# Kernel tuning notes

Measured on AMD Instinct MI355X. Metric: run time of the kernel, lower is better.

The kernel has to match this reference:

```python
import jax, jax.numpy as jnp
import numpy as np

B, N, D, H = 1, 4096, 768, 12
HD = D // H
SCALE = HD ** -0.5

def setup_inputs() -> dict:
    key = jax.random.key(0)
    k1, k2, k3 = jax.random.split(key, 3)
    x = jax.random.normal(k1, (B, N, D), dtype=jnp.float32)
    W_qkv = jax.random.normal(k2, (D, 3 * D), dtype=jnp.float32) * (D ** -0.5)
    W_out = jax.random.normal(k3, (D, D), dtype=jnp.float32) * (D ** -0.5)
    b_out = jnp.zeros((D,), dtype=jnp.float32)
    return {"x": x, "W_qkv": W_qkv, "W_out": W_out, "b_out": b_out}

def reference(x, W_qkv, W_out, b_out):
    # qkv projection: (B,N,3D)
    qkv = x @ W_qkv
    q, k, v = jnp.split(qkv, 3, axis=-1)
    # (B,N,D) -> (B,H,N,hd)
    def heads(t):
        return t.reshape(B, N, H, HD).transpose(0, 2, 1, 3)
    q, k, v = heads(q), heads(k), heads(v)
    scores = jnp.einsum('bhnd,bhmd->bhnm', q, k) * SCALE  # (B,H,N,N)
    attn = jax.nn.softmax(scores, axis=-1)
    out = jnp.einsum('bhnm,bhmd->bhnd', attn, v)
    out = out.transpose(0, 2, 1, 3).reshape(B, N, D)
    return out @ W_out + b_out
```

## Files before the change

kernel.cpp:

```cpp
#include <hip/hip_runtime.h>
#include <hip/hip_bf16.h>
#include <math.h>

typedef __attribute__((ext_vector_type(8))) short bf16x8;
typedef __attribute__((ext_vector_type(4))) short bf16x4;
typedef __attribute__((ext_vector_type(4))) float floatx4;

constexpr int kN  = 4096;
constexpr int kD  = 768;
constexpr int kH  = 12;
constexpr int kHD = 64;
constexpr int k3D = 2304;
constexpr float kQScale = 0.18033688011112042f;

static __device__ __forceinline__ short f2b(float f) {
    __hip_bfloat16 h = __float2bfloat16(f);
    return *reinterpret_cast<short*>(&h);
}

static __device__ __forceinline__ float fast_exp2(float x) {
#if __has_builtin(__builtin_amdgcn_exp2f)
    return __builtin_amdgcn_exp2f(x);
#else
    return exp2f(x);
#endif
}

static __device__ __forceinline__ void async_copy16(const void* g, void* l) {
    __builtin_amdgcn_global_load_lds(
        (const __attribute__((address_space(1))) void*)g,
        (__attribute__((address_space(3))) void*)l, 16, 0, 0);
}

constexpr int kBlkX  = 1536;
constexpr int kBlkWq = 72 * 24;
constexpr int kBlkWo = 24 * 24;

__global__ __launch_bounds__(256)
void prep(const float* __restrict__ x, const float* __restrict__ Wq,
          const float* __restrict__ Wo, short* __restrict__ Xb,
          short* __restrict__ WqT, short* __restrict__ WoT)
{
    const int bid = blockIdx.x;
    const int tid = threadIdx.x;
    if (bid < kBlkX) {
        const int i = bid * 256 + tid;
        const float4* s = reinterpret_cast<const float4*>(x + (size_t)i * 8);
        float4 a = s[0], b = s[1];
        bf16x8 v;
        v[0] = f2b(a.x); v[1] = f2b(a.y); v[2] = f2b(a.z); v[3] = f2b(a.w);
        v[4] = f2b(b.x); v[5] = f2b(b.y); v[6] = f2b(b.z); v[7] = f2b(b.w);
        *reinterpret_cast<bf16x8*>(Xb + (size_t)i * 8) = v;
        return;
    }
    const float* src; short* dst; int R, C, bx, by;
    if (bid < kBlkX + kBlkWq) {
        const int local = bid - kBlkX;
        src = Wq; dst = WqT; R = kD; C = k3D; bx = local % 72; by = local / 72;
    } else {
        const int local = bid - kBlkX - kBlkWq;
        src = Wo; dst = WoT; R = kD; C = kD; bx = local % 24; by = local / 24;
    }
    __shared__ float t[32][33];
    const int c0 = bx * 32, r0 = by * 32;
    const int tx = tid & 31, ty = tid >> 5;
    #pragma unroll
    for (int i = ty; i < 32; i += 8)
        t[i][tx] = src[(size_t)(r0 + i) * C + c0 + tx];
    __syncthreads();
    #pragma unroll
    for (int i = ty; i < 32; i += 8)
        dst[(size_t)(c0 + i) * R + r0 + tx] = f2b(t[tx][i]);
}

template<int MODE>
__device__ __forceinline__
void gemm_core(const short* __restrict__ A, const short* __restrict__ BT,
               const float* __restrict__ bias, float* __restrict__ Cout,
               short* __restrict__ Qh, short* __restrict__ Kh, short* __restrict__ Vt,
               int N, int K)
{
    const int bm   = blockIdx.x * 128;
    const int bn   = blockIdx.y * 128;
    const int tid  = threadIdx.x;
    const int wave = tid >> 6;
    const int lane = tid & 63;
    const int l15  = lane & 15;
    const int quad = lane >> 4;
    const int l3   = l15 & 3;

    __shared__ alignas(16) short As[128 * 32];
    __shared__ alignas(16) short Bs[128 * 32];

    floatx4 acc[4][4] = {};
    const int wm = (wave >> 1) * 64;
    const int wn = (wave & 1) * 64;

    const int srl = lane >> 2;
    const int scc = (lane & 3) ^ (srl & 3);

    for (int k0 = 0; k0 < K; k0 += 32) {
        __syncthreads();
        #pragma unroll
        for (int j = 0; j < 2; ++j) {
            const int rs = 32 * wave + 16 * j;
            async_copy16(&A [(size_t)(bm + rs + srl) * K + k0 + 8 * scc], &As[rs * 32]);
            async_copy16(&BT[(size_t)(bn + rs + srl) * K + k0 + 8 * scc], &Bs[rs * 32]);
        }
        __syncthreads();

        bf16x8 af[4], bfr[4];
        #pragma unroll
        for (int mt = 0; mt < 4; ++mt)
            af[mt] = *reinterpret_cast<const bf16x8*>(&As[(wm + 16 * mt + l15) * 32 + 8 * (quad ^ l3)]);
        #pragma unroll
        for (int nt = 0; nt < 4; ++nt)
            bfr[nt] = *reinterpret_cast<const bf16x8*>(&Bs[(wn + 16 * nt + l15) * 32 + 8 * (quad ^ l3)]);
        #pragma unroll
        for (int mt = 0; mt < 4; ++mt)
            #pragma unroll
            for (int nt = 0; nt < 4; ++nt)
                acc[mt][nt] = __builtin_amdgcn_mfma_f32_16x16x32_bf16(af[mt], bfr[nt], acc[mt][nt], 0, 0, 0);
    }

    #pragma unroll
    for (int mt = 0; mt < 4; ++mt) {
        #pragma unroll
        for (int nt = 0; nt < 4; ++nt) {
            #pragma unroll
            for (int r = 0; r < 4; ++r) {
                const int row = bm + wm + mt * 16 + 4 * quad + r;
                const int col = bn + wn + nt * 16 + l15;
                float v = acc[mt][nt][r];
                if (MODE == 0) {
                    Cout[(size_t)row * N + col] = v + bias[col];
                } else {
                    const int proj   = col / kD;
                    const int within = col - proj * kD;
                    const int h = within >> 6;
                    const int d = within & 63;
                    if (proj == 0)      Qh[((size_t)h * kN + row) * kHD + d] = f2b(v * kQScale);
                    else if (proj == 1) Kh[((size_t)h * kN + row) * kHD + d] = f2b(v);
                    else                Vt[((size_t)h * kHD + d) * kN + row] = f2b(v);
                }
            }
        }
    }
}

__global__ __launch_bounds__(256)
void gemm_qkv(const short* __restrict__ A, const short* __restrict__ BT,
              short* __restrict__ Qh, short* __restrict__ Kh, short* __restrict__ Vt)
{
    gemm_core<1>(A, BT, nullptr, nullptr, Qh, Kh, Vt, k3D, kD);
}

__global__ __launch_bounds__(256)
void gemm_out(const short* __restrict__ A, const short* __restrict__ BT,
              const float* __restrict__ bias, float* __restrict__ Cout)
{
    gemm_core<0>(A, BT, bias, Cout, nullptr, nullptr, nullptr, kD, kD);
}

__global__ __launch_bounds__(256)
void attn(const short* __restrict__ Qh, const short* __restrict__ Kh,
          const short* __restrict__ Vt, short* __restrict__ AO)
{
    const int h    = blockIdx.y;
    const int q0   = blockIdx.x * 64;
    const int tid  = threadIdx.x;
    const int wave = tid >> 6;
    const int lane = tid & 63;
    const int l15  = lane & 15;
    const int quad = lane >> 4;
    const int lx   = l15 & 7;

    __shared__ alignas(16) short Ks[2][64 * 64];
    __shared__ alignas(16) short Vs[2][64 * 64];
    __shared__ alignas(16) short Pm[4][16 * 64];

    const int qrow = q0 + 16 * wave + l15;
    const size_t qbase = ((size_t)h * kN + qrow) * kHD;
    bf16x8 qf[2];
    qf[0] = *reinterpret_cast<const bf16x8*>(&Qh[qbase + quad * 8]);
    qf[1] = *reinterpret_cast<const bf16x8*>(&Qh[qbase + 32 + quad * 8]);

    bf16x8 onesf;
    #pragma unroll
    for (int i = 0; i < 8; ++i) onesf[i] = (short)0x3F80;

    floatx4 oacc[4] = {};
    floatx4 dacc = {};

    const int srl = lane >> 3;
    const int scc = (lane & 7) ^ srl;

    short* Pw = Pm[wave];

    const size_t kbase = (size_t)h * kN * kHD;
    const size_t vbase = (size_t)h * kHD * kN;

    auto stage = [&](int b, int kv0) {
        #pragma unroll
        for (int j = 0; j < 2; ++j) {
            const int r0 = 16 * wave + 8 * j;
            async_copy16(&Kh[kbase + (size_t)(kv0 + r0 + srl) * kHD + 8 * scc],
                         &Ks[b][r0 * 64]);
            async_copy16(&Vt[vbase + (size_t)(r0 + srl) * kN + kv0 + 8 * scc],
                         &Vs[b][r0 * 64]);
        }
    };

    constexpr int kNT = kN / 64;
    int cur = 0;
    stage(0, 0);

    for (int t = 0; t < kNT; ++t) {
        __syncthreads();
        if (t + 1 < kNT) stage(cur ^ 1, (t + 1) * 64);

        const short* Kc = Ks[cur];
        const short* Vc = Vs[cur];

        floatx4 sacc[4] = {};
        __builtin_amdgcn_s_setprio(1);
        #pragma unroll
        for (int nt = 0; nt < 4; ++nt) {
            #pragma unroll
            for (int s = 0; s < 2; ++s) {
                bf16x8 kf = *reinterpret_cast<const bf16x8*>(
                    &Kc[(16 * nt + l15) * 64 + 8 * ((4 * s + quad) ^ lx)]);
                sacc[nt] = __builtin_amdgcn_mfma_f32_16x16x32_bf16(kf, qf[s], sacc[nt], 0, 0, 0);
            }
        }
        __builtin_amdgcn_s_setprio(0);

        #pragma unroll
        for (int nt = 0; nt < 4; ++nt) {
            const float p0 = fast_exp2(sacc[nt][0]);
            const float p1 = fast_exp2(sacc[nt][1]);
            const float p2 = fast_exp2(sacc[nt][2]);
            const float p3 = fast_exp2(sacc[nt][3]);
            bf16x4 pk;
            pk[0] = f2b(p0); pk[1] = f2b(p1); pk[2] = f2b(p2); pk[3] = f2b(p3);
            const int c = 2 * nt + (quad >> 1);
            *reinterpret_cast<bf16x4*>(
                &Pw[l15 * 64 + 8 * (c ^ lx) + 4 * (quad & 1)]) = pk;
        }

        __builtin_amdgcn_s_setprio(1);
        #pragma unroll
        for (int s = 0; s < 2; ++s) {
            bf16x8 pa = *reinterpret_cast<const bf16x8*>(
                &Pw[l15 * 64 + 8 * ((4 * s + quad) ^ lx)]);
            dacc = __builtin_amdgcn_mfma_f32_16x16x32_bf16(pa, onesf, dacc, 0, 0, 0);
            #pragma unroll
            for (int dt = 0; dt < 4; ++dt) {
                bf16x8 vv = *reinterpret_cast<const bf16x8*>(
                    &Vc[(16 * dt + l15) * 64 + 8 * ((4 * s + quad) ^ lx)]);
                oacc[dt] = __builtin_amdgcn_mfma_f32_16x16x32_bf16(pa, vv, oacc[dt], 0, 0, 0);
            }
        }
        __builtin_amdgcn_s_setprio(0);

        cur ^= 1;
    }

    float inv[4];
    #pragma unroll
    for (int r = 0; r < 4; ++r) inv[r] = 1.0f / dacc[r];

    #pragma unroll
    for (int dt = 0; dt < 4; ++dt) {
        #pragma unroll
        for (int r = 0; r < 4; ++r) {
            const int row = q0 + 16 * wave + 4 * quad + r;
            const int col = h * kHD + 16 * dt + l15;
            AO[(size_t)row * kD + col] = f2b(oacc[dt][r] * inv[r]);
        }
    }
}

extern "C" void kernel_launch(void* const* d_in, const int* in_sizes, int n_in,
                              void* d_out, int out_size, void* d_ws, size_t ws_size,
                              hipStream_t stream)
{
    const float* x     = (const float*)d_in[0];
    const float* W_qkv = (const float*)d_in[1];
    const float* W_out = (const float*)d_in[2];
    const float* b_out = (const float*)d_in[3];
    float* out = (float*)d_out;

    const size_t HNHD = (size_t)kH * kN * kHD;
    short* Qh    = (short*)d_ws;
    short* Kh    = Qh + HNHD;
    short* Vt    = Kh + HNHD;
    short* Xb    = Vt + HNHD;
    short* WqkvT = Xb + (size_t)kN * kD;
    short* WoutT = WqkvT + (size_t)k3D * kD;
    short* AO    = Xb;
    (void)in_sizes; (void)n_in; (void)out_size; (void)ws_size;

    prep<<<dim3(kBlkX + kBlkWq + kBlkWo), dim3(256), 0, stream>>>(
        x, W_qkv, W_out, Xb, WqkvT, WoutT);

    gemm_qkv<<<dim3(kN / 128, k3D / 128), dim3(256), 0, stream>>>(
        Xb, WqkvT, Qh, Kh, Vt);
    attn<<<dim3(kN / 64, kH), dim3(256), 0, stream>>>(Qh, Kh, Vt, AO);
    gemm_out<<<dim3(kN / 128, kD / 128), dim3(256), 0, stream>>>(
        AO, WoutT, b_out, out);
}
```

Baseline: 200.8 us.

## Use two waves per attention block with 32 query rows each and remap blocks

The attention kernel now runs 128 threads per block, and each wave handles two 16-row query tiles. This lets every K and V fragment read from LDS feed two MFMAs instead of one, halving LDS traffic per FLOP. Block indices are remapped so consecutive blocks spread across heads, likely for L2/XCD locality. It also interleaves exp with QK per key tile. In exchange it uses more registers per wave and has fewer waves per block to hide latency.

```diff
diff --git a/kernel.cpp b/kernel.cpp
--- a/kernel.cpp
+++ b/kernel.cpp
@@ -162,12 +162,15 @@
     gemm_core<0>(A, BT, bias, Cout, nullptr, nullptr, nullptr, kD, kD);
 }
 
-__global__ __launch_bounds__(256)
+__global__ __launch_bounds__(128)
 void attn(const short* __restrict__ Qh, const short* __restrict__ Kh,
           const short* __restrict__ Vt, short* __restrict__ AO)
 {
-    const int h    = blockIdx.y;
-    const int q0   = blockIdx.x * 64;
+    const int flat = blockIdx.y * 64 + blockIdx.x;
+    const int W    = (flat & 7) * 96 + (flat >> 3);
+    const int h    = W >> 6;
+    const int q0   = (W & 63) * 64;
+
     const int tid  = threadIdx.x;
     const int wave = tid >> 6;
     const int lane = tid & 63;
@@ -177,20 +180,25 @@
 
     __shared__ alignas(16) short Ks[2][64 * 64];
     __shared__ alignas(16) short Vs[2][64 * 64];
-    __shared__ alignas(16) short Pm[4][16 * 64];
-
-    const int qrow = q0 + 16 * wave + l15;
-    const size_t qbase = ((size_t)h * kN + qrow) * kHD;
-    bf16x8 qf[2];
-    qf[0] = *reinterpret_cast<const bf16x8*>(&Qh[qbase + quad * 8]);
-    qf[1] = *reinterpret_cast<const bf16x8*>(&Qh[qbase + 32 + quad * 8]);
+    __shared__ alignas(16) short Pm[2][32 * 64];
+
+    bf16x8 qf[2][2];
+    {
+        const size_t qb = ((size_t)h * kN + q0 + 32 * wave + l15) * kHD;
+        #pragma unroll
+        for (int mt = 0; mt < 2; ++mt)
+            #pragma unroll
+            for (int s = 0; s < 2; ++s)
+                qf[mt][s] = *reinterpret_cast<const bf16x8*>(
+                    &Qh[qb + (size_t)(16 * mt) * kHD + 32 * s + 8 * quad]);
+    }
 
     bf16x8 onesf;
     #pragma unroll
     for (int i = 0; i < 8; ++i) onesf[i] = (short)0x3F80;
 
-    floatx4 oacc[4] = {};
-    floatx4 dacc = {};
+    floatx4 oacc[2][4] = {};
+    floatx4 dacc[2] = {};
 
     const int srl = lane >> 3;
     const int scc = (lane & 7) ^ srl;
@@ -202,8 +210,8 @@
 
     auto stage = [&](int b, int kv0) {
         #pragma unroll
-        for (int j = 0; j < 2; ++j) {
-            const int r0 = 16 * wave + 8 * j;
+        for (int j = 0; j < 4; ++j) {
+            const int r0 = 32 * wave + 8 * j;
             async_copy16(&Kh[kbase + (size_t)(kv0 + r0 + srl) * kHD + 8 * scc],
                          &Ks[b][r0 * 64]);
             async_copy16(&Vt[vbase + (size_t)(r0 + srl) * kN + kv0 + 8 * scc],
@@ -222,61 +230,71 @@
         const short* Kc = Ks[cur];
         const short* Vc = Vs[cur];
 
-        floatx4 sacc[4] = {};
+        #pragma unroll
+        for (int nt = 0; nt < 4; ++nt) {
+            bf16x8 kf0 = *reinterpret_cast<const bf16x8*>(
+                &Kc[(16 * nt + l15) * 64 + 8 * ((quad) ^ lx)]);
+            bf16x8 kf1 = *reinterpret_cast<const bf16x8*>(
+                &Kc[(16 * nt + l15) * 64 + 8 * ((4 + quad) ^ lx)]);
+            floatx4 sacc[2] = {};
+            __builtin_amdgcn_s_setprio(1);
+            #pragma unroll
+            for (int mt = 0; mt < 2; ++mt) {
+                sacc[mt] = __builtin_amdgcn_mfma_f32_16x16x32_bf16(kf0, qf[mt][0], sacc[mt], 0, 0, 0);
+                sacc[mt] = __builtin_amdgcn_mfma_f32_16x16x32_bf16(kf1, qf[mt][1], sacc[mt], 0, 0, 0);
+            }
+            __builtin_amdgcn_s_setprio(0);
+            #pragma unroll
+            for (int mt = 0; mt < 2; ++mt) {
+                const float p0 = fast_exp2(sacc[mt][0]);
+                const float p1 = fast_exp2(sacc[mt][1]);
+                const float p2 = fast_exp2(sacc[mt][2]);
+                const float p3 = fast_exp2(sacc[mt][3]);
+                bf16x4 pk;
+                pk[0] = f2b(p0); pk[1] = f2b(p1); pk[2] = f2b(p2); pk[3] = f2b(p3);
+                const int c = 2 * nt + (quad >> 1);
+                *reinterpret_cast<bf16x4*>(
+                    &Pw[mt * 1024 + l15 * 64 + 8 * (c ^ lx) + 4 * (quad & 1)]) = pk;
+            }
+        }
+
         __builtin_amdgcn_s_setprio(1);
         #pragma unroll
-        for (int nt = 0; nt < 4; ++nt) {
-            #pragma unroll
-            for (int s = 0; s < 2; ++s) {
-                bf16x8 kf = *reinterpret_cast<const bf16x8*>(
-                    &Kc[(16 * nt + l15) * 64 + 8 * ((4 * s + quad) ^ lx)]);
-                sacc[nt] = __builtin_amdgcn_mfma_f32_16x16x32_bf16(kf, qf[s], sacc[nt], 0, 0, 0);
+        for (int s = 0; s < 2; ++s) {
+            bf16x8 vv[4];
+            #pragma unroll
+            for (int dt = 0; dt < 4; ++dt)
+                vv[dt] = *reinterpret_cast<const bf16x8*>(
+                    &Vc[(16 * dt + l15) * 64 + 8 * ((4 * s + quad) ^ lx)]);
+            #pragma unroll
+            for (int mt = 0; mt < 2; ++mt) {
+                bf16x8 pa = *reinterpret_cast<const bf16x8*>(
+                    &Pw[mt * 1024 + l15 * 64 + 8 * ((4 * s + quad) ^ lx)]);
+                dacc[mt] = __builtin_amdgcn_mfma_f32_16x16x32_bf16(pa, onesf, dacc[mt], 0, 0, 0);
+                #pragma unroll
+                for (int dt = 0; dt < 4; ++dt)
+                    oacc[mt][dt] = __builtin_amdgcn_mfma_f32_16x16x32_bf16(
+                        pa, vv[dt], oacc[mt][dt], 0, 0, 0);
             }
         }
         __builtin_amdgcn_s_setprio(0);
 
-        #pragma unroll
-        for (int nt = 0; nt < 4; ++nt) {
-            const float p0 = fast_exp2(sacc[nt][0]);
-            const float p1 = fast_exp2(sacc[nt][1]);
-            const float p2 = fast_exp2(sacc[nt][2]);
-            const float p3 = fast_exp2(sacc[nt][3]);
-            bf16x4 pk;
-            pk[0] = f2b(p0); pk[1] = f2b(p1); pk[2] = f2b(p2); pk[3] = f2b(p3);
-            const int c = 2 * nt + (quad >> 1);
-            *reinterpret_cast<bf16x4*>(
-                &Pw[l15 * 64 + 8 * (c ^ lx) + 4 * (quad & 1)]) = pk;
-        }
-
-        __builtin_amdgcn_s_setprio(1);
-        #pragma unroll
-        for (int s = 0; s < 2; ++s) {
-            bf16x8 pa = *reinterpret_cast<const bf16x8*>(
-                &Pw[l15 * 64 + 8 * ((4 * s + quad) ^ lx)]);
-            dacc = __builtin_amdgcn_mfma_f32_16x16x32_bf16(pa, onesf, dacc, 0, 0, 0);
-            #pragma unroll
-            for (int dt = 0; dt < 4; ++dt) {
-                bf16x8 vv = *reinterpret_cast<const bf16x8*>(
-                    &Vc[(16 * dt + l15) * 64 + 8 * ((4 * s + quad) ^ lx)]);
-                oacc[dt] = __builtin_amdgcn_mfma_f32_16x16x32_bf16(pa, vv, oacc[dt], 0, 0, 0);
-            }
-        }
-        __builtin_amdgcn_s_setprio(0);
-
         cur ^= 1;
     }
 
-    float inv[4];
-    #pragma unroll
-    for (int r = 0; r < 4; ++r) inv[r] = 1.0f / dacc[r];
-
-    #pragma unroll
-    for (int dt = 0; dt < 4; ++dt) {
-        #pragma unroll
-        for (int r = 0; r < 4; ++r) {
-            const int row = q0 + 16 * wave + 4 * quad + r;
-            const int col = h * kHD + 16 * dt + l15;
-            AO[(size_t)row * kD + col] = f2b(oacc[dt][r] * inv[r]);
+    #pragma unroll
+    for (int mt = 0; mt < 2; ++mt) {
+        float inv[4];
+        #pragma unroll
+        for (int r = 0; r < 4; ++r) inv[r] = 1.0f / dacc[mt][r];
+        #pragma unroll
+        for (int dt = 0; dt < 4; ++dt) {
+            #pragma unroll
+            for (int r = 0; r < 4; ++r) {
+                const int row = q0 + 32 * wave + 16 * mt + 4 * quad + r;
+                const int col = h * kHD + 16 * dt + l15;
+                AO[(size_t)row * kD + col] = f2b(oacc[mt][dt][r] * inv[r]);
+            }
         }
     }
 }
@@ -306,7 +324,7 @@
 
     gemm_qkv<<<dim3(kN / 128, k3D / 128), dim3(256), 0, stream>>>(
         Xb, WqkvT, Qh, Kh, Vt);
-    attn<<<dim3(kN / 64, kH), dim3(256), 0, stream>>>(Qh, Kh, Vt, AO);
+    attn<<<dim3(kN / 64, kH), dim3(128), 0, stream>>>(Qh, Kh, Vt, AO);
     gemm_out<<<dim3(kN / 128, kD / 128), dim3(256), 0, stream>>>(
         AO, WoutT, b_out, out);
 }
```

After: 217.6 us. +8.4%, slower.
